# Performance work log

Measured on AMD Instinct MI355X. Metric: run time of the kernel, lower is better.

Reference implementation:

```python
import jax, jax.numpy as jnp
import numpy as np

B, C, H, W = 4, 320, 32, 32
HEADS = 8
LTXT, DCROSS = 77, 768
HW = H * W


def _ln(x, w, b, eps=1e-5):
    mu = x.mean(-1, keepdims=True)
    var = jnp.var(x, axis=-1, keepdims=True)
    return (x - mu) * jax.lax.rsqrt(var + eps) * w + b


def _gn(x, w, b, groups=32, eps=1e-6):
    Bx, Cx, Hx, Wx = x.shape
    xg = x.reshape(Bx, groups, -1)
    mu = xg.mean(-1, keepdims=True)
    var = jnp.var(xg, axis=-1, keepdims=True)
    xn = ((xg - mu) * jax.lax.rsqrt(var + eps)).reshape(Bx, Cx, Hx, Wx)
    return xn * w[None, :, None, None] + b[None, :, None, None]


def _attn(q, k, v, bias=None):
    Bq, S, Cd = q.shape
    dh = Cd // HEADS
    qh = q.reshape(Bq, S, HEADS, dh)
    kh = k.reshape(Bq, -1, HEADS, dh)
    vh = v.reshape(Bq, -1, HEADS, dh)
    s = jnp.einsum('bqhd,bkhd->bhqk', qh, kh) * (1.0 / np.sqrt(dh))
    if bias is not None:
        s = s + bias  # additive 0/1 otsu mask, exactly as the torch code passes it
    p = jax.nn.softmax(s, axis=-1)
    o = jnp.einsum('bhqk,bkhd->bqhd', p, vh).reshape(Bq, S, Cd)
    return o, p


def _block(x, ctx, prm, bias=None):
    # BasicTransformerBlock: self-attn -> cross-attn (returns probs) -> GEGLU FF
    (ln1w, ln1b, qkv, ow, ob, ln2w, ln2b, q2, kv2, o2w, o2b,
     ln3w, ln3b, ff1w, ff1b, ff2w, ff2b) = prm
    h = _ln(x, ln1w, ln1b)
    q, k, v = jnp.split(h @ qkv, 3, axis=-1)
    o, _ = _attn(q, k, v)
    x = x + o @ ow + ob
    h = _ln(x, ln2w, ln2b)
    k2, v2 = jnp.split(ctx @ kv2, 2, axis=-1)
    o2, p2 = _attn(h @ q2, k2, v2, bias)
    x = x + o2 @ o2w + o2b
    h = _ln(x, ln3w, ln3b)
    a, g = jnp.split(h @ ff1w + ff1b, 2, axis=-1)
    x = x + (a * jax.nn.gelu(g)) @ ff2w + ff2b
    return x, p2


def _otsu(m):
    # vectorized version of the 10-threshold otsu loop (m: [B/2, N])
    mn = m.min(-1, keepdims=True)
    mx = m.max(-1, keepdims=True)
    x = (m - mn) / (mx - mn)
    n = x.shape[-1]
    ts = jnp.arange(10, dtype=x.dtype) * 0.1  # thresholds t*0.1
    low = x[:, None, :] < ts[None, :, None]   # [B/2, 10, N]
    cnt_low = low.sum(-1).astype(x.dtype)
    cnt_high = n - cnt_low
    sum_low = jnp.where(low, x[:, None, :], 0.0).sum(-1)
    sum_high = x.sum(-1, keepdims=True) - sum_low
    mu_low = jnp.where(cnt_low > 0, sum_low / jnp.maximum(cnt_low, 1.0), jnp.nan)
    mu_high = jnp.where(cnt_high > 0, sum_high / jnp.maximum(cnt_high, 1.0), jnp.nan)
    g = (cnt_low / n) * (cnt_high / n) * (mu_low - mu_high) ** 2
    g = jnp.where(jnp.isnan(g), -jnp.inf, g)  # torch: nan > max_g is False -> skipped
    best = jnp.argmax(g, axis=-1)             # first max == torch strict-> ties keep earliest
    gmax = jnp.take_along_axis(g, best[:, None], axis=-1)[:, 0]
    thr = jnp.where(gmax > 0, best.astype(x.dtype) * 0.1, 0.0)[:, None]
    return jnp.where(x < thr, 0.0, jnp.where(x > thr, 1.0, x))


def _fwd(gn_w, gn_b, pin_w, pin_b,
         b_ln1w, b_ln1b, b_qkv, b_ow, b_ob, b_ln2w, b_ln2b, b_q2, b_kv2, b_o2w, b_o2b,
         b_ln3w, b_ln3b, b_ff1w, b_ff1b, b_ff2w, b_ff2b,
         i_ln1w, i_ln1b, i_qkv, i_ow, i_ob, i_ln2w, i_ln2b, i_q2, i_kv2, i_o2w, i_o2b,
         i_ln3w, i_ln3b, i_ff1w, i_ff1b, i_ff2w, i_ff2b,
         pout_w, pout_b, hidden_states, encoder_hidden_states,
         ph_b, ph_t, eot_b, eot_t):
    residual = hidden_states
    h = _gn(hidden_states, gn_w, gn_b)
    h = h.transpose(0, 2, 3, 1).reshape(B, HW, C)
    h = h @ pin_w + pin_b  # use_linear_projection path
    blk = (b_ln1w, b_ln1b, b_qkv, b_ow, b_ob, b_ln2w, b_ln2b, b_q2, b_kv2, b_o2w, b_o2b,
           b_ln3w, b_ln3b, b_ff1w, b_ff1b, b_ff2w, b_ff2b)
    iblk = (i_ln1w, i_ln1b, i_qkv, i_ow, i_ob, i_ln2w, i_ln2b, i_q2, i_kv2, i_o2w, i_o2b,
            i_ln3w, i_ln3b, i_ff1w, i_ff1b, i_ff2w, i_ff2b)
    h, probs = _block(h, encoder_hidden_states, blk)   # probs [B, heads, HW, 77]
    ap = probs.mean(1)[B // 2:]                        # head-avg attn_probs, cond half
    attn = ap.transpose(0, 2, 1)                       # [B/2, 77, HW]
    attn_ph = attn[ph_b, ph_t]                         # [B/2, HW]
    attn_eot = jax.lax.stop_gradient(attn[eot_b, eot_t])
    loss_reg = jnp.mean((attn_ph / attn_ph.max(-1, keepdims=True)
                         - attn_eot / attn_eot.max(-1, keepdims=True)) ** 2)
    mask = _otsu(jax.lax.stop_gradient(attn_ph))       # [B/2, HW]
    bias = mask[:, None, None, :]                      # broadcast over heads and queries
    hs, img = h[:B // 2], h[B // 2:]
    hs, _ = _block(hs, img, iblk, bias)                # image_cross_attention
    h = jnp.concatenate([hs, img], axis=0)
    h = h @ pout_w + pout_b
    sample = h.reshape(B, H, W, C).transpose(0, 3, 1, 2) + residual
    return sample, loss_reg


def setup_inputs():
    key = jax.random.key(0)
    ki = iter(jax.random.split(key, 80))
    f32 = jnp.float32

    def rn(shape, s=0.02):
        return jax.random.normal(next(ki), shape, f32) * s

    def blk(p, cross):
        return {p + 'ln1w': jnp.ones((C,), f32), p + 'ln1b': jnp.zeros((C,), f32),
                p + 'qkv': rn((C, 3 * C)), p + 'ow': rn((C, C)), p + 'ob': jnp.zeros((C,), f32),
                p + 'ln2w': jnp.ones((C,), f32), p + 'ln2b': jnp.zeros((C,), f32),
                p + 'q2': rn((C, C)), p + 'kv2': rn((cross, 2 * C)),
                p + 'o2w': rn((C, C)), p + 'o2b': jnp.zeros((C,), f32),
                p + 'ln3w': jnp.ones((C,), f32), p + 'ln3b': jnp.zeros((C,), f32),
                p + 'ff1w': rn((C, 8 * C)), p + 'ff1b': jnp.zeros((8 * C,), f32),
                p + 'ff2w': rn((4 * C, C)), p + 'ff2b': jnp.zeros((C,), f32)}

    inp = {'gn_w': jnp.ones((C,), f32), 'gn_b': jnp.zeros((C,), f32),
           'pin_w': rn((C, C)), 'pin_b': jnp.zeros((C,), f32)}
    inp.update(blk('b_', DCROSS))
    inp.update(blk('i_', C))
    inp['pout_w'] = rn((C, C))
    inp['pout_b'] = jnp.zeros((C,), f32)
    inp['hidden_states'] = jax.random.normal(next(ki), (B, C, H, W), f32)
    inp['encoder_hidden_states'] = jax.random.normal(next(ki), (B, LTXT, DCROSS), f32)
    inp['ph_b'] = jnp.arange(B // 2)
    inp['ph_t'] = jax.random.randint(next(ki), (B // 2,), 0, LTXT)
    inp['eot_b'] = jnp.arange(B // 2)
    inp['eot_t'] = jax.random.randint(next(ki), (B // 2,), 0, LTXT)
    return inp


def reference(gn_w, gn_b, pin_w, pin_b,
              b_ln1w, b_ln1b, b_qkv, b_ow, b_ob, b_ln2w, b_ln2b, b_q2, b_kv2, b_o2w, b_o2b,
              b_ln3w, b_ln3b, b_ff1w, b_ff1b, b_ff2w, b_ff2b,
              i_ln1w, i_ln1b, i_qkv, i_ow, i_ob, i_ln2w, i_ln2b, i_q2, i_kv2, i_o2w, i_o2b,
              i_ln3w, i_ln3b, i_ff1w, i_ff1b, i_ff2w, i_ff2b,
              pout_w, pout_b, hidden_states, encoder_hidden_states,
              ph_b, ph_t, eot_b, eot_t):
    return _fwd(gn_w, gn_b, pin_w, pin_b,
                b_ln1w, b_ln1b, b_qkv, b_ow, b_ob, b_ln2w, b_ln2b, b_q2, b_kv2, b_o2w, b_o2b,
                b_ln3w, b_ln3b, b_ff1w, b_ff1b, b_ff2w, b_ff2b,
                i_ln1w, i_ln1b, i_qkv, i_ow, i_ob, i_ln2w, i_ln2b, i_q2, i_kv2, i_o2w, i_o2b,
                i_ln3w, i_ln3b, i_ff1w, i_ff1b, i_ff2w, i_ff2b,
                pout_w, pout_b, hidden_states, encoder_hidden_states,
                ph_b, ph_t, eot_b, eot_t)
```

## Files before the change

### kernel.cpp

```cpp
#include <hip/hip_runtime.h>
#include <hip/hip_bf16.h>
#include <math.h>

#define NH 8
#define DH 40
#define CCH 320
#define SCALE 0.15811388300841897f

typedef __attribute__((ext_vector_type(8))) short short8;
typedef __attribute__((ext_vector_type(4))) float float4v;

static __device__ __forceinline__ unsigned short f2bf(float x) {
  __hip_bfloat16 t = __float2bfloat16(x);
  return *reinterpret_cast<unsigned short*>(&t);
}

static __device__ __forceinline__ void gload16(const void* g, void* l) {
  __builtin_amdgcn_global_load_lds((__attribute__((address_space(1))) void*)g,
                                   (__attribute__((address_space(3))) void*)l, 16, 0, 0);
}

__global__ __launch_bounds__(256) void gn_kernel(const float* __restrict__ x,
                                                 const float* __restrict__ w,
                                                 const float* __restrict__ b,
                                                 unsigned short* __restrict__ out) {
  int batch = blockIdx.x >> 5;
  int g = blockIdx.x & 31;
  const int CPG = 10;
  const float* xp = x + ((size_t)batch * CCH + g * CPG) * 1024;
  float s = 0.f, ss = 0.f;
  for (int i = threadIdx.x; i < CPG * 1024; i += 256) { float v = xp[i]; s += v; ss += v * v; }
  __shared__ float r1[256], r2[256];
  r1[threadIdx.x] = s; r2[threadIdx.x] = ss; __syncthreads();
  for (int off = 128; off > 0; off >>= 1) {
    if (threadIdx.x < off) { r1[threadIdx.x] += r1[threadIdx.x + off]; r2[threadIdx.x] += r2[threadIdx.x + off]; }
    __syncthreads();
  }
  float mu = r1[0] * (1.f / 10240.f);
  float var = r2[0] * (1.f / 10240.f) - mu * mu;
  float inv = rsqrtf(var + 1e-6f);
  for (int i = threadIdx.x; i < CPG * 1024; i += 256) {
    int ci = i >> 10; int hw = i & 1023; int c = g * CPG + ci;
    float v = (xp[i] - mu) * inv * w[c] + b[c];
    out[((size_t)batch * 1024 + hw) * CCH + c] = f2bf(v);
  }
}

__global__ __launch_bounds__(256) void ln_kernel(const float* __restrict__ x,
                                                 const float* __restrict__ w,
                                                 const float* __restrict__ b,
                                                 unsigned short* __restrict__ out, int M) {
  int row = blockIdx.x * 4 + (threadIdx.x >> 6);
  if (row >= M) return;
  const float* xp = x + (size_t)row * CCH;
  int lane = threadIdx.x & 63;
  float v[5]; float s = 0.f;
#pragma unroll
  for (int i = 0; i < 5; i++) { v[i] = xp[lane + 64 * i]; s += v[i]; }
#pragma unroll
  for (int o = 32; o > 0; o >>= 1) s += __shfl_xor(s, o);
  float mu = s * (1.f / 320.f);
  float ss = 0.f;
#pragma unroll
  for (int i = 0; i < 5; i++) { float d = v[i] - mu; ss += d * d; }
#pragma unroll
  for (int o = 32; o > 0; o >>= 1) ss += __shfl_xor(ss, o);
  float inv = rsqrtf(ss * (1.f / 320.f) + 1e-5f);
  unsigned short* op = out + (size_t)row * CCH;
#pragma unroll
  for (int i = 0; i < 5; i++) { int c = lane + 64 * i; op[c] = f2bf((v[i] - mu) * inv * w[c] + b[c]); }
}

struct WTab {
  const float* src[16];
  unsigned short* dst[16];
  int Kd[16];
  int Nd[16];
  int perm[16];
  int tstart[17];
  float* lz;
};
__global__ __launch_bounds__(256) void wconv_kernel(WTab t) {
  __shared__ float tile[32][33];
  if (blockIdx.x == 0 && threadIdx.x == 0) *t.lz = 0.f;
  int gid = blockIdx.x;
  int w = 0;
  while (w < 15 && gid >= t.tstart[w + 1]) w++;
  int local = gid - t.tstart[w];
  int K = t.Kd[w], N = t.Nd[w];
  int ntx = (N + 31) >> 5;
  int bx = local % ntx, by = local / ntx;
  int nb = bx * 32, kb = by * 32;
  const float* src = t.src[w];
  unsigned short* dst = t.dst[w];
  int doperm = t.perm[w];
  int half = N >> 1;
  int tx = threadIdx.x & 31, ty = threadIdx.x >> 5;
  for (int i = ty; i < 32; i += 8) {
    int k = kb + i, n = nb + tx;
    tile[i][tx] = (k < K && n < N) ? src[(size_t)k * N + n] : 0.f;
  }
  __syncthreads();
  for (int i = ty; i < 32; i += 8) {
    int n = nb + i, k = kb + tx;
    if (n < N && k < K) {
      int nd = n;
      if (doperm) {
        if (n < half) nd = (n >> 5) * 64 + (n & 31);
        else { int c = n - half; nd = (c >> 5) * 64 + 32 + (c & 31); }
      }
      dst[(size_t)nd * K + k] = f2bf(tile[tx][i]);
    }
  }
}

__global__ __launch_bounds__(256) void lngemm64_kernel(const float* __restrict__ A,
                                                       const float* __restrict__ lnw,
                                                       const float* __restrict__ lnb,
                                                       const unsigned short* __restrict__ Bt,
                                                       unsigned short* __restrict__ outp,
                                                       int M, int N) {
  __shared__ unsigned short As[64][328];
  __shared__ unsigned short Bsd[2][64][32];
  __shared__ float Wf[320], Bf[320];
  __shared__ float Mu[64], Iv[64];
  const int K = 320;
  int tid = threadIdx.x;
  int lane = tid & 63;
  int wv = tid >> 6;
  int quad = lane >> 4;
  int col = lane & 15;
  int m0 = blockIdx.y * 64;
  int n0 = blockIdx.x * 64;
  const unsigned short* bp0 = Bt + (size_t)(n0 + (tid >> 2)) * K + (tid & 3) * 8;
  gload16(bp0, ((char*)Bsd[0]) + wv * 1024);
  for (int i = tid; i < 320; i += 256) { Wf[i] = lnw[i]; Bf[i] = lnb[i]; }
  int l32 = tid & 31;
  int rsub = tid >> 5;
  for (int it = 0; it < 8; it++) {
    int r = it * 8 + rsub;
    const float* ap = A + (size_t)(m0 + r) * K;
    float s = 0.f, ss = 0.f;
#pragma unroll
    for (int j = 0; j < 10; j++) { float v = ap[l32 + j * 32]; s += v; ss += v * v; }
#pragma unroll
    for (int o = 16; o > 0; o >>= 1) { s += __shfl_xor(s, o); ss += __shfl_xor(ss, o); }
    if (l32 == 0) {
      float mu = s * (1.f / 320.f);
      Mu[r] = mu;
      Iv[r] = rsqrtf(ss * (1.f / 320.f) - mu * mu + 1e-5f);
    }
  }
  __syncthreads();
#pragma unroll 4
  for (int i = 0; i < 20; i++) {
    int cc = i * 256 + tid;
    int r = cc / 80, c4 = cc - r * 80;
    int c = c4 * 4;
    float4 v = *(const float4*)(A + (size_t)(m0 + r) * K + c);
    float mu = Mu[r], iv = Iv[r];
    ushort4 o;
    o.x = f2bf((v.x - mu) * iv * Wf[c] + Bf[c]);
    o.y = f2bf((v.y - mu) * iv * Wf[c + 1] + Bf[c + 1]);
    o.z = f2bf((v.z - mu) * iv * Wf[c + 2] + Bf[c + 2]);
    o.w = f2bf((v.w - mu) * iv * Wf[c + 3] + Bf[c + 3]);
    *(ushort4*)&As[r][c] = o;
  }
  __syncthreads();
  float4v acc[4];
  float4v zero = {0.f, 0.f, 0.f, 0.f};
#pragma unroll
  for (int j = 0; j < 4; j++) acc[j] = zero;
  for (int t = 0; t < 10; t++) {
    if (t < 9) gload16(bp0 + (t + 1) * 32, ((char*)Bsd[(t + 1) & 1]) + wv * 1024);
    int k0 = t * 32;
    short8 af = *(short8*)&As[wv * 16 + col][k0 + quad * 8];
#pragma unroll
    for (int j = 0; j < 4; j++) {
      short8 bfr = *(short8*)&Bsd[t & 1][j * 16 + col][quad * 8];
      acc[j] = __builtin_amdgcn_mfma_f32_16x16x32_bf16(af, bfr, acc[j], 0, 0, 0);
    }
    __syncthreads();
  }
#pragma unroll
  for (int j = 0; j < 4; j++) {
    int n = n0 + j * 16 + col;
#pragma unroll
    for (int r = 0; r < 4; r++) {
      int m = m0 + wv * 16 + quad * 4 + r;
      outp[(size_t)m * N + n] = f2bf(acc[j][r]);
    }
  }
}

__global__ __launch_bounds__(256) void mergegemm64_kernel(const float* __restrict__ Opart,
                                                          const float* __restrict__ mpart,
                                                          const float* __restrict__ lpart,
                                                          const unsigned short* __restrict__ Bt,
                                                          const float* __restrict__ bias,
                                                          float* __restrict__ h, int M) {
  __shared__ unsigned short As[64][328];
  __shared__ unsigned short Bsd[2][64][32];
  const int K = 320;
  int tid = threadIdx.x;
  int lane = tid & 63;
  int wv = tid >> 6;
  int quad = lane >> 4;
  int col = lane & 15;
  int m0 = blockIdx.y * 64;
  int n0 = blockIdx.x * 64;
  const unsigned short* bp0 = Bt + (size_t)(n0 + (tid >> 2)) * K + (tid & 3) * 8;
  gload16(bp0, ((char*)Bsd[0]) + wv * 1024);
#pragma unroll
  for (int i = 0; i < 10; i++) {
    int cc = i * 256 + tid;
    int r = cc / 40, c8 = cc - r * 40;
    int c = c8 * 8;
    int hh = c / 40;
    int d = c - hh * 40;
    int m = m0 + r, b = m >> 10, q = m & 1023;
    size_t ri = ((size_t)(b * NH + hh) * 1024 + q) * 4;
    float ma = mpart[ri], mb = mpart[ri + 1], mc = mpart[ri + 2], md = mpart[ri + 3];
    float Mx = fmaxf(fmaxf(ma, mb), fmaxf(mc, md));
    float w0 = __expf(ma - Mx), w1 = __expf(mb - Mx), w2 = __expf(mc - Mx), w3 = __expf(md - Mx);
    float L = lpart[ri] * w0 + lpart[ri + 1] * w1 + lpart[ri + 2] * w2 + lpart[ri + 3] * w3;
    float inv = 1.f / L;
    w0 *= inv; w1 *= inv; w2 *= inv; w3 *= inv;
    const float* p0 = Opart + (ri + 0) * DH + d;
    const float* p1 = Opart + (ri + 1) * DH + d;
    const float* p2 = Opart + (ri + 2) * DH + d;
    const float* p3 = Opart + (ri + 3) * DH + d;
    float4 a0 = *(const float4*)p0, a1 = *(const float4*)p1, a2 = *(const float4*)p2, a3 = *(const float4*)p3;
    float4 b0 = *(const float4*)(p0 + 4), b1 = *(const float4*)(p1 + 4), b2 = *(const float4*)(p2 + 4), b3 = *(const float4*)(p3 + 4);
    ushort4 u0, u1;
    u0.x = f2bf(a0.x * w0 + a1.x * w1 + a2.x * w2 + a3.x * w3);
    u0.y = f2bf(a0.y * w0 + a1.y * w1 + a2.y * w2 + a3.y * w3);
    u0.z = f2bf(a0.z * w0 + a1.z * w1 + a2.z * w2 + a3.z * w3);
    u0.w = f2bf(a0.w * w0 + a1.w * w1 + a2.w * w2 + a3.w * w3);
    u1.x = f2bf(b0.x * w0 + b1.x * w1 + b2.x * w2 + b3.x * w3);
    u1.y = f2bf(b0.y * w0 + b1.y * w1 + b2.y * w2 + b3.y * w3);
    u1.z = f2bf(b0.z * w0 + b1.z * w1 + b2.z * w2 + b3.z * w3);
    u1.w = f2bf(b0.w * w0 + b1.w * w1 + b2.w * w2 + b3.w * w3);
    *(ushort4*)&As[r][c] = u0;
    *(ushort4*)&As[r][c + 4] = u1;
  }
  __syncthreads();
  float4v acc[4];
  float4v zero = {0.f, 0.f, 0.f, 0.f};
#pragma unroll
  for (int j = 0; j < 4; j++) acc[j] = zero;
  for (int t = 0; t < 10; t++) {
    if (t < 9) gload16(bp0 + (t + 1) * 32, ((char*)Bsd[(t + 1) & 1]) + wv * 1024);
    int k0 = t * 32;
    short8 af = *(short8*)&As[wv * 16 + col][k0 + quad * 8];
#pragma unroll
    for (int j = 0; j < 4; j++) {
      short8 bfr = *(short8*)&Bsd[t & 1][j * 16 + col][quad * 8];
      acc[j] = __builtin_amdgcn_mfma_f32_16x16x32_bf16(af, bfr, acc[j], 0, 0, 0);
    }
    __syncthreads();
  }
#pragma unroll
  for (int j = 0; j < 4; j++) {
    int n = n0 + j * 16 + col;
    float bv = bias[n];
#pragma unroll
    for (int r = 0; r < 4; r++) {
      int m = m0 + wv * 16 + quad * 4 + r;
      size_t oi = (size_t)m * 320 + n;
      h[oi] = acc[j][r] + bv + h[oi];
    }
  }
}

__global__ __launch_bounds__(256) void mgemm64_kernel(const void* __restrict__ Ap,
                                                      const unsigned short* __restrict__ Bt,
                                                      const float* __restrict__ bias,
                                                      const float* __restrict__ res,
                                                      void* __restrict__ outp,
                                                      void* __restrict__ outp2,
                                                      int M, int N, int K, int a32, int omode) {
  __shared__ unsigned short As[64][160];
  __shared__ unsigned short Bs[64][160];
  int tid = threadIdx.x;
  int lane = tid & 63;
  int wv = tid >> 6;
  int quad = lane >> 4;
  int col = lane & 15;
  int m0 = blockIdx.y * 64;
  int n0 = blockIdx.x * 64;
  float4v acc[4];
  float4v zero = {0.f, 0.f, 0.f, 0.f};
#pragma unroll
  for (int j = 0; j < 4; j++) acc[j] = zero;
  short8 vzero = {0, 0, 0, 0, 0, 0, 0, 0};
  int kfast = (!a32) && ((K % 160) == 0);
  int off[5];
#pragma unroll
  for (int i = 0; i < 5; i++) { int c = i * 256 + tid; int row = c / 20; off[i] = row * K + (c - row * 20) * 8; }
  int wb = (tid & 192) * 16;
  const unsigned short* Ab = (const unsigned short*)Ap + (size_t)m0 * K;
  const unsigned short* Bb = Bt + (size_t)n0 * K;
  for (int k0 = 0; k0 < K; k0 += 160) {
    if (kfast) {
#pragma unroll
      for (int i = 0; i < 5; i++) {
        gload16(Ab + off[i] + k0, ((char*)As) + wb + i * 4096);
        gload16(Bb + off[i] + k0, ((char*)Bs) + wb + i * 4096);
      }
    } else {
#pragma unroll
      for (int i = 0; i < 5; i++) {
        int u = tid + i * 256;
        int row = u / 20, seg = u - row * 20;
        int k = k0 + seg * 8;
        int m = m0 + row;
        short8 av = vzero;
        if (m < M && k < K) {
          if (a32) {
            const float* Af = (const float*)Ap;
            float4 f0 = *(const float4*)(Af + (size_t)m * K + k);
            float4 f1 = *(const float4*)(Af + (size_t)m * K + k + 4);
            av[0] = (short)f2bf(f0.x); av[1] = (short)f2bf(f0.y);
            av[2] = (short)f2bf(f0.z); av[3] = (short)f2bf(f0.w);
            av[4] = (short)f2bf(f1.x); av[5] = (short)f2bf(f1.y);
            av[6] = (short)f2bf(f1.z); av[7] = (short)f2bf(f1.w);
          } else {
            av = *(const short8*)((const unsigned short*)Ap + (size_t)m * K + k);
          }
        }
        *(short8*)&As[row][seg * 8] = av;
        int n = n0 + row;
        short8 bv = vzero;
        if (n < N && k < K) bv = *(const short8*)(Bt + (size_t)n * K + k);
        *(short8*)&Bs[row][seg * 8] = bv;
      }
    }
    __syncthreads();
#pragma unroll
    for (int kk = 0; kk < 5; kk++) {
      int kq2 = kk * 32 + quad * 8;
      short8 af = *(short8*)&As[wv * 16 + col][kq2];
#pragma unroll
      for (int j = 0; j < 4; j++) {
        short8 bfr = *(short8*)&Bs[j * 16 + col][kq2];
        acc[j] = __builtin_amdgcn_mfma_f32_16x16x32_bf16(af, bfr, acc[j], 0, 0, 0);
      }
    }
    __syncthreads();
  }
  if (omode == 3) {
    int half = N >> 1;
#pragma unroll
    for (int jb = 0; jb < 2; jb++) {
      int nout = (n0 >> 1) + jb * 16 + col;
      float ba = bias[nout];
      float bg = bias[half + nout];
#pragma unroll
      for (int r = 0; r < 4; r++) {
        int m = m0 + wv * 16 + quad * 4 + r;
        if (m < M) {
          float a = acc[jb][r] + ba;
          float g = acc[jb + 2][r] + bg;
          float t2 = tanhf(0.7978845608028654f * (g + 0.044715f * g * g * g));
          ((unsigned short*)outp)[(size_t)m * half + nout] = f2bf(a * (0.5f * g * (1.f + t2)));
        }
      }
    }
    return;
  }
#pragma unroll
  for (int j = 0; j < 4; j++) {
    int n = n0 + j * 16 + col;
    if (n >= N) continue;
    float bv = bias ? bias[n] : 0.f;
#pragma unroll
    for (int r = 0; r < 4; r++) {
      int m = m0 + wv * 16 + quad * 4 + r;
      if (m < M) {
        float v = acc[j][r] + bv;
        if (omode == 2) {
          int bq = m >> 10, hw = m & 1023;
          size_t oi = ((size_t)bq * N + n) * 1024 + hw;
          ((float*)outp)[oi] = v + res[oi];
        } else {
          if (res) v += res[(size_t)m * N + n];
          if (omode == 1) ((unsigned short*)outp)[(size_t)m * N + n] = f2bf(v);
          else {
            ((float*)outp)[(size_t)m * N + n] = v;
            if (omode == 4) ((unsigned short*)outp2)[(size_t)m * N + n] = f2bf(v);
          }
        }
      }
    }
  }
}

#define VSTR 72
__global__ __launch_bounds__(256) void mfattns_kernel(const unsigned short* __restrict__ qp, int qstr,
                                                      const unsigned short* __restrict__ kp, int kstr,
                                                      const unsigned short* __restrict__ vp, int vstr,
                                                      const float* __restrict__ bias,
                                                      float* __restrict__ Opart,
                                                      float* __restrict__ mpart,
                                                      float* __restrict__ lpart) {
  __shared__ unsigned short Ks[64 * 56];
  __shared__ unsigned short Vt[48 * VSTR];
  __shared__ unsigned short Ps[4][16 * 72];
  int tid = threadIdx.x;
  int lane = tid & 63;
  int wv = tid >> 6;
  int quad = lane >> 4;
  int col = lane & 15;
  int bid = blockIdx.x;
  int split = bid & 3;
  int qt = (bid >> 2) & 15;
  int h = (bid >> 6) & 7;
  int b = bid >> 9;

  short8 zero8 = {0, 0, 0, 0, 0, 0, 0, 0};
  int qrow = qt * 64 + wv * 16 + col;
  const unsigned short* qbase = qp + (size_t)(b * 1024 + qrow) * qstr + h * DH;
  short8 qf0 = *(const short8*)(qbase + quad * 8);
  short8 qf1 = (quad == 0) ? *(const short8*)(qbase + 32) : zero8;

  float4v Oacc[3];
  float4v fzero = {0.f, 0.f, 0.f, 0.f};
  Oacc[0] = fzero; Oacc[1] = fzero; Oacc[2] = fzero;
  float mr[4] = {-3.4e38f, -3.4e38f, -3.4e38f, -3.4e38f};
  float lr[4] = {0.f, 0.f, 0.f, 0.f};

  for (int kt = split * 4; kt < split * 4 + 4; kt++) {
    int kb = kt * 64;
    __syncthreads();
    for (int u = tid; u < 384; u += 256) {
      int key = u / 6, s = u - key * 6;
      short8 kv8 = zero8;
      if (s < 5) kv8 = *(const short8*)(kp + (size_t)(b * 1024 + kb + key) * kstr + h * DH + s * 8);
      *(short8*)&Ks[key * 56 + s * 8] = kv8;
    }
    for (int u = tid; u < 384; u += 256) {
      int s = u >> 6, key = u & 63;
      short8 vv8 = zero8;
      if (s < 5) vv8 = *(const short8*)(vp + (size_t)(b * 1024 + kb + key) * vstr + h * DH + s * 8);
#pragma unroll
      for (int j = 0; j < 8; j++) Vt[(s * 8 + j) * VSTR + key] = (unsigned short)vv8[j];
    }
    __syncthreads();

    float4v sf[4];
#pragma unroll
    for (int jb = 0; jb < 4; jb++) {
      const unsigned short* krow = &Ks[(jb * 16 + col) * 56];
      short8 bk0 = *(const short8*)(krow + quad * 8);
      short8 bk1 = (quad == 0) ? *(const short8*)(krow + 32) : zero8;
      float4v s = fzero;
      s = __builtin_amdgcn_mfma_f32_16x16x32_bf16(qf0, bk0, s, 0, 0, 0);
      s = __builtin_amdgcn_mfma_f32_16x16x32_bf16(qf1, bk1, s, 0, 0, 0);
      float bv = bias ? bias[b * 1024 + kb + jb * 16 + col] : 0.f;
#pragma unroll
      for (int r = 0; r < 4; r++) s[r] = s[r] * SCALE + bv;
      sf[jb] = s;
    }
    float tmax[4];
#pragma unroll
    for (int r = 0; r < 4; r++) {
      float t = fmaxf(fmaxf(sf[0][r], sf[1][r]), fmaxf(sf[2][r], sf[3][r]));
#pragma unroll
      for (int o = 1; o < 16; o <<= 1) t = fmaxf(t, __shfl_xor(t, o));
      tmax[r] = t;
    }
    float al[4];
#pragma unroll
    for (int r = 0; r < 4; r++) {
      float mnew = fmaxf(mr[r], tmax[r]);
      al[r] = __expf(mr[r] - mnew);
      mr[r] = mnew;
      lr[r] *= al[r];
    }
#pragma unroll
    for (int nb = 0; nb < 3; nb++)
#pragma unroll
      for (int r = 0; r < 4; r++) Oacc[nb][r] *= al[r];
    float rs[4] = {0.f, 0.f, 0.f, 0.f};
#pragma unroll
    for (int jb = 0; jb < 4; jb++) {
#pragma unroll
      for (int r = 0; r < 4; r++) {
        float p = __expf(sf[jb][r] - mr[r]);
        rs[r] += p;
        Ps[wv][(quad * 4 + r) * 72 + jb * 16 + col] = f2bf(p);
      }
    }
#pragma unroll
    for (int r = 0; r < 4; r++) {
      float t = rs[r];
#pragma unroll
      for (int o = 1; o < 16; o <<= 1) t += __shfl_xor(t, o);
      lr[r] += t;
    }
#pragma unroll
    for (int kc = 0; kc < 2; kc++) {
      int koff = kc * 32 + quad * 8;
      short8 pa = *(const short8*)&Ps[wv][col * 72 + koff];
#pragma unroll
      for (int nb = 0; nb < 3; nb++) {
        short8 vb = *(const short8*)&Vt[(nb * 16 + col) * VSTR + koff];
        Oacc[nb] = __builtin_amdgcn_mfma_f32_16x16x32_bf16(pa, vb, Oacc[nb], 0, 0, 0);
      }
    }
  }
#pragma unroll
  for (int r = 0; r < 4; r++) {
    int qo = qt * 64 + wv * 16 + quad * 4 + r;
    size_t rowidx = (size_t)(b * NH + h) * 1024 + qo;
    float* orow = Opart + (rowidx * 4 + split) * DH;
#pragma unroll
    for (int nb = 0; nb < 3; nb++) {
      int d = nb * 16 + col;
      if (d < DH) orow[d] = Oacc[nb][r];
    }
    if (col == 0) {
      mpart[rowidx * 4 + split] = mr[r];
      lpart[rowidx * 4 + split] = lr[r];
    }
  }
}

#define CVSTR 104
__global__ __launch_bounds__(256) void cattnm_kernel(const unsigned short* __restrict__ qp,
                                                     const unsigned short* __restrict__ kvp,
                                                     unsigned short* __restrict__ op,
                                                     float* __restrict__ probs) {
  __shared__ unsigned short Ks[80 * 56];
  __shared__ unsigned short Vt[48 * CVSTR];
  __shared__ unsigned short Ps[4][16 * 104];
  int tid = threadIdx.x;
  int lane = tid & 63;
  int wv = tid >> 6;
  int quad = lane >> 4;
  int col = lane & 15;
  int bid = blockIdx.x;
  int qt = bid & 15;
  int h = (bid >> 4) & 7;
  int b = bid >> 7;

  short8 zero8 = {0, 0, 0, 0, 0, 0, 0, 0};
  for (int u = tid; u < 480; u += 256) {
    int key = u / 6, s = u - key * 6;
    short8 v8 = zero8;
    if (s < 5 && key < 77) v8 = *(const short8*)(kvp + (size_t)(b * 77 + key) * 640 + h * DH + s * 8);
    *(short8*)&Ks[key * 56 + s * 8] = v8;
  }
  for (int u = tid; u < 576; u += 256) {
    int s = u / 96, key = u - s * 96;
    short8 v8 = zero8;
    if (s < 5 && key < 77) v8 = *(const short8*)(kvp + (size_t)(b * 77 + key) * 640 + 320 + h * DH + s * 8);
#pragma unroll
    for (int j = 0; j < 8; j++) Vt[(s * 8 + j) * CVSTR + key] = (unsigned short)v8[j];
  }
  int qrow = qt * 64 + wv * 16 + col;
  const unsigned short* qbase = qp + (size_t)(b * 1024 + qrow) * CCH + h * DH;
  short8 qf0 = *(const short8*)(qbase + quad * 8);
  short8 qf1 = (quad == 0) ? *(const short8*)(qbase + 32) : zero8;
  __syncthreads();

  float4v fzero = {0.f, 0.f, 0.f, 0.f};
  float4v sf[5];
#pragma unroll
  for (int jb = 0; jb < 5; jb++) {
    const unsigned short* krow = &Ks[(jb * 16 + col) * 56];
    short8 bk0 = *(const short8*)(krow + quad * 8);
    short8 bk1 = (quad == 0) ? *(const short8*)(krow + 32) : zero8;
    float4v s = fzero;
    s = __builtin_amdgcn_mfma_f32_16x16x32_bf16(qf0, bk0, s, 0, 0, 0);
    s = __builtin_amdgcn_mfma_f32_16x16x32_bf16(qf1, bk1, s, 0, 0, 0);
    int key = jb * 16 + col;
    float msk = (key < 77) ? 0.f : -3.4e38f;
#pragma unroll
    for (int r = 0; r < 4; r++) s[r] = s[r] * SCALE + msk;
    sf[jb] = s;
  }
  float inv[4];
#pragma unroll
  for (int r = 0; r < 4; r++) {
    float t = sf[0][r];
#pragma unroll
    for (int jb = 1; jb < 5; jb++) t = fmaxf(t, sf[jb][r]);
#pragma unroll
    for (int o = 1; o < 16; o <<= 1) t = fmaxf(t, __shfl_xor(t, o));
    float sum = 0.f;
#pragma unroll
    for (int jb = 0; jb < 5; jb++) { float e = __expf(sf[jb][r] - t); sf[jb][r] = e; sum += e; }
#pragma unroll
    for (int o = 1; o < 16; o <<= 1) sum += __shfl_xor(sum, o);
    inv[r] = 1.f / sum;
  }
#pragma unroll
  for (int jb = 0; jb < 5; jb++) {
    int key = jb * 16 + col;
    float4v pv;
#pragma unroll
    for (int r = 0; r < 4; r++) {
      float p = sf[jb][r] * inv[r];
      Ps[wv][(quad * 4 + r) * 104 + jb * 16 + col] = f2bf(p);
      pv[r] = p;
    }
    if (b >= 2 && key < 77) {
      size_t pi = ((size_t)((b - 2) * NH + h) * 77 + key) * 1024 + qt * 64 + wv * 16 + quad * 4;
      *(float4v*)&probs[pi] = pv;
    }
  }
  float4v Oacc[3];
  Oacc[0] = fzero; Oacc[1] = fzero; Oacc[2] = fzero;
#pragma unroll
  for (int kc = 0; kc < 3; kc++) {
    int koff = kc * 32 + quad * 8;
    short8 pa = (koff < 80) ? *(const short8*)&Ps[wv][col * 104 + koff] : zero8;
#pragma unroll
    for (int nb = 0; nb < 3; nb++) {
      short8 vb = *(const short8*)&Vt[(nb * 16 + col) * CVSTR + koff];
      Oacc[nb] = __builtin_amdgcn_mfma_f32_16x16x32_bf16(pa, vb, Oacc[nb], 0, 0, 0);
    }
  }
#pragma unroll
  for (int r = 0; r < 4; r++) {
    int qo = qt * 64 + wv * 16 + quad * 4 + r;
    unsigned short* orow = op + (size_t)(b * 1024 + qo) * CCH + h * DH;
#pragma unroll
    for (int nb = 0; nb < 3; nb++) {
      int d = nb * 16 + col;
      if (d < DH) orow[d] = f2bf(Oacc[nb][r]);
    }
  }
}

__global__ __launch_bounds__(256) void eol_kernel(const float* __restrict__ pT,
                                                  const int* __restrict__ phb, const int* __restrict__ pht,
                                                  const int* __restrict__ eob, const int* __restrict__ eot,
                                                  float* __restrict__ mask,
                                                  float* __restrict__ lossout) {
  __shared__ float S[4][24];
  __shared__ float shthr;
  int i = blockIdx.x, tid = threadIdx.x;
  int lane = tid & 63, wv = tid >> 6;
  int pb = phb[i], pt = pht[i], eb = eob[i], et = eot[i];
  float x[4], y[4];
#pragma unroll
  for (int j = 0; j < 4; j++) {
    int q = tid + 256 * j;
    float s1 = 0.f, s2 = 0.f;
#pragma unroll
    for (int hh = 0; hh < NH; hh++) {
      s1 += pT[((size_t)(pb * NH + hh) * 77 + pt) * 1024 + q];
      s2 += pT[((size_t)(eb * NH + hh) * 77 + et) * 1024 + q];
    }
    x[j] = s1 * 0.125f;
    y[j] = s2 * 0.125f;
  }
  float mx = fmaxf(fmaxf(x[0], x[1]), fmaxf(x[2], x[3]));
  float me = fmaxf(fmaxf(y[0], y[1]), fmaxf(y[2], y[3]));
  float mn = fminf(fminf(x[0], x[1]), fminf(x[2], x[3]));
  float sx = x[0] + x[1] + x[2] + x[3];
#pragma unroll
  for (int o = 32; o > 0; o >>= 1) {
    mx = fmaxf(mx, __shfl_xor(mx, o));
    me = fmaxf(me, __shfl_xor(me, o));
    mn = fminf(mn, __shfl_xor(mn, o));
    sx += __shfl_xor(sx, o);
  }
  if (lane == 0) { S[wv][0] = mx; S[wv][1] = me; S[wv][2] = mn; S[wv][3] = sx; }
  __syncthreads();
  mx = fmaxf(fmaxf(S[0][0], S[1][0]), fmaxf(S[2][0], S[3][0]));
  me = fmaxf(fmaxf(S[0][1], S[1][1]), fmaxf(S[2][1], S[3][1]));
  mn = fminf(fminf(S[0][2], S[1][2]), fminf(S[2][2], S[3][2]));
  sx = S[0][3] + S[1][3] + S[2][3] + S[3][3];
  float invmp = 1.f / mx, invme = 1.f / me;
  float inv = 1.f / (mx - mn);
  float lp = 0.f;
  float cnt[10], sm[10];
#pragma unroll
  for (int t = 0; t < 10; t++) { cnt[t] = 0.f; sm[t] = 0.f; }
#pragma unroll
  for (int j = 0; j < 4; j++) {
    float d = x[j] * invmp - y[j] * invme;
    lp += d * d;
    float v = (x[j] - mn) * inv;
#pragma unroll
    for (int t = 0; t < 10; t++) {
      if (v < t * 0.1f) { cnt[t] += 1.f; sm[t] += v; }
    }
  }
#pragma unroll
  for (int o = 32; o > 0; o >>= 1) {
    lp += __shfl_xor(lp, o);
#pragma unroll
    for (int t = 0; t < 10; t++) { cnt[t] += __shfl_xor(cnt[t], o); sm[t] += __shfl_xor(sm[t], o); }
  }
  __syncthreads();
  if (lane == 0) {
    S[wv][0] = lp;
#pragma unroll
    for (int t = 0; t < 10; t++) { S[wv][1 + t] = cnt[t]; S[wv][11 + t] = sm[t]; }
  }
  __syncthreads();
  if (tid == 0) {
    float lpt = S[0][0] + S[1][0] + S[2][0] + S[3][0];
    atomicAdd(lossout, lpt * (1.f / 2048.f));
    float total = (sx - 1024.f * mn) * inv;
    float gmax = -3.4e38f; int best = 0;
    for (int t = 0; t < 10; t++) {
      float c_low = S[0][1 + t] + S[1][1 + t] + S[2][1 + t] + S[3][1 + t];
      float s_low = S[0][11 + t] + S[1][11 + t] + S[2][11 + t] + S[3][11 + t];
      float c_high = 1024.f - c_low;
      float g;
      if (c_low > 0.f && c_high > 0.f) {
        float mu_l = s_low / c_low;
        float mu_h = (total - s_low) / c_high;
        float dd = mu_l - mu_h;
        g = (c_low * (1.f / 1024.f)) * (c_high * (1.f / 1024.f)) * dd * dd;
      } else g = -3.4e38f;
      if (g > gmax) { gmax = g; best = t; }
    }
    shthr = (gmax > 0.f) ? best * 0.1f : 0.f;
  }
  __syncthreads();
  float thr = shthr;
#pragma unroll
  for (int j = 0; j < 4; j++) {
    int q = tid + 256 * j;
    float v = (x[j] - mn) * inv;
    mask[i * 1024 + q] = (v < thr) ? 0.f : ((v > thr) ? 1.f : v);
  }
}

extern "C" void kernel_launch(void* const* d_in, const int* in_sizes, int n_in,
                              void* d_out, int out_size, void* d_ws, size_t ws_size,
                              hipStream_t stream) {
  auto F = [&](int i) { return (const float*)d_in[i]; };
  auto I = [&](int i) { return (const int*)d_in[i]; };

  float* ws = (float*)d_ws;
  float* h    = ws;
  float* ffb  = h    + 1310720;
  float* p2   = ffb  + 10485760;
  float* mask = p2   + 2523136;

  float* Opart = ffb;
  float* mpart = ffb + 5242880;
  float* lpart = ffb + 5242880 + 131072;

  unsigned short* b16   = (unsigned short*)(mask + 2048);
  unsigned short* lnb16 = b16;
  unsigned short* attb16= lnb16 + 1310720;
  unsigned short* actb16= attb16 + 1310720;
  unsigned short* qkv16 = actb16 + 5242880;
  unsigned short* q16   = qkv16 + 3932160;
  unsigned short* kv16  = q16 + 1310720;
  unsigned short* hb16  = kv16 + 1310720;
  unsigned short* wptr  = hb16 + 1310720;

  auto walloc = [&](int n) { unsigned short* p = wptr; wptr += n; return p; };
  unsigned short* pin_t  = walloc(102400);
  unsigned short* bqkv_t = walloc(307200);
  unsigned short* bow_t  = walloc(102400);
  unsigned short* bq2_t  = walloc(102400);
  unsigned short* bkv2_t = walloc(491520);
  unsigned short* bo2_t  = walloc(102400);
  unsigned short* bff1_t = walloc(819200);
  unsigned short* bff2_t = walloc(409600);
  unsigned short* iqkv_t = walloc(307200);
  unsigned short* iow_t  = walloc(102400);
  unsigned short* iq2_t  = walloc(102400);
  unsigned short* ikv2_t = walloc(204800);
  unsigned short* io2_t  = walloc(102400);
  unsigned short* iff1_t = walloc(819200);
  unsigned short* iff2_t = walloc(409600);
  unsigned short* pout_t = walloc(102400);

  float* out = (float*)d_out;

  WTab wt;
  wt.lz = out + 1310720;
  int nt = 0, cnt = 0;
  auto addw = [&](const float* s, unsigned short* d, int K, int N, int perm) {
    wt.src[cnt] = s; wt.dst[cnt] = d; wt.Kd[cnt] = K; wt.Nd[cnt] = N; wt.perm[cnt] = perm;
    wt.tstart[cnt] = nt;
    nt += ((K + 31) / 32) * ((N + 31) / 32);
    cnt++;
  };
  addw(F(2), pin_t, 320, 320, 0);
  addw(F(4 + 2), bqkv_t, 320, 960, 0);
  addw(F(4 + 3), bow_t, 320, 320, 0);
  addw(F(4 + 7), bq2_t, 320, 320, 0);
  addw(F(4 + 8), bkv2_t, 768, 640, 0);
  addw(F(4 + 9), bo2_t, 320, 320, 0);
  addw(F(4 + 13), bff1_t, 320, 2560, 1);
  addw(F(4 + 15), bff2_t, 1280, 320, 0);
  addw(F(21 + 2), iqkv_t, 320, 960, 0);
  addw(F(21 + 3), iow_t, 320, 320, 0);
  addw(F(21 + 7), iq2_t, 320, 320, 0);
  addw(F(21 + 8), ikv2_t, 320, 640, 0);
  addw(F(21 + 9), io2_t, 320, 320, 0);
  addw(F(21 + 13), iff1_t, 320, 2560, 1);
  addw(F(21 + 15), iff2_t, 1280, 320, 0);
  addw(F(38), pout_t, 320, 320, 0);
  wt.tstart[16] = nt;

  wconv_kernel<<<nt, 256, 0, stream>>>(wt);

  auto gemm64 = [&](const void* A, const unsigned short* Wt, const float* bias,
                    const float* res, void* o, int M, int N, int K, int a32, int omode,
                    void* o2 = nullptr) {
    dim3 g((N + 63) / 64, (M + 63) / 64);
    mgemm64_kernel<<<g, 256, 0, stream>>>(A, Wt, bias, res, o, o2, M, N, K, a32, omode);
  };
  auto lngemm = [&](const float* A, const float* lw, const float* lb,
                    const unsigned short* Wt, unsigned short* o, int M, int N) {
    dim3 g(N / 64, M / 64);
    lngemm64_kernel<<<g, 256, 0, stream>>>(A, lw, lb, Wt, o, M, N);
  };
  auto mergegemm = [&](const unsigned short* Wt, const float* bias, int M) {
    dim3 g(5, M / 64);
    mergegemm64_kernel<<<g, 256, 0, stream>>>(Opart, mpart, lpart, Wt, bias, h, M);
  };

  gn_kernel<<<128, 256, 0, stream>>>(F(40), F(0), F(1), lnb16);
  gemm64(lnb16, pin_t, F(3), nullptr, h, 4096, 320, 320, 0, 0);

  auto run_block = [&](int p, int Bx, bool img_block,
                       const unsigned short* qkv_t, const unsigned short* ow_t,
                       const unsigned short* q2_t, const unsigned short* kv2_t,
                       const unsigned short* o2_t, const unsigned short* ff1_t,
                       const unsigned short* ff2_t) {
    int M = Bx * 1024;
    ln_kernel<<<M / 4, 256, 0, stream>>>(h, F(p + 0), F(p + 1), lnb16, M);
    gemm64(lnb16, qkv_t, nullptr, nullptr, qkv16, M, 960, 320, 0, 1);
    mfattns_kernel<<<Bx * 512, 256, 0, stream>>>(qkv16, 960, qkv16 + 320, 960, qkv16 + 640, 960,
                                                 nullptr, Opart, mpart, lpart);
    mergegemm(ow_t, F(p + 4), M);
    lngemm(h, F(p + 5), F(p + 6), q2_t, q16, M, 320);
    if (!img_block) {
      gemm64(F(41), kv2_t, nullptr, nullptr, kv16, Bx * 77, 640, 768, 1, 1);
      cattnm_kernel<<<Bx * 128, 256, 0, stream>>>(q16, kv16, attb16, p2);
      gemm64(attb16, o2_t, F(p + 10), h, h, M, 320, 320, 0, 0);
    } else {
      gemm64(hb16 + (size_t)2 * 1024 * 320, kv2_t, nullptr, nullptr, kv16, Bx * 1024, 640, 320, 0, 1);
      mfattns_kernel<<<Bx * 512, 256, 0, stream>>>(q16, 320, kv16, 640, kv16 + 320, 640,
                                                   mask, Opart, mpart, lpart);
      mergegemm(o2_t, F(p + 10), M);
    }
    ln_kernel<<<M / 4, 256, 0, stream>>>(h, F(p + 11), F(p + 12), lnb16, M);
    gemm64(lnb16, ff1_t, F(p + 14), nullptr, actb16, M, 2560, 320, 0, 3);
    gemm64(actb16, ff2_t, F(p + 16), h, h, M, 320, 1280, 0, 4, hb16);
  };

  run_block(4, 4, false, bqkv_t, bow_t, bq2_t, bkv2_t, bo2_t, bff1_t, bff2_t);

  eol_kernel<<<2, 256, 0, stream>>>(p2, I(42), I(43), I(44), I(45), mask, out + 1310720);

  run_block(21, 2, true, iqkv_t, iow_t, iq2_t, ikv2_t, io2_t, iff1_t, iff2_t);

  gemm64(hb16, pout_t, F(39), F(40), out, 4096, 320, 320, 0, 2);
}
```

Measured before the change: 527.8 us.

## Use base-2 softmax with lazy rescaling and split merge from out-projection GEMM

```diff
diff --git a/kernel.cpp b/kernel.cpp
--- a/kernel.cpp
+++ b/kernel.cpp
@@ -6,6 +6,8 @@
 #define DH 40
 #define CCH 320
 #define SCALE 0.15811388300841897f
+#define SCL2 0.22810857f
+#define LOG2E 1.44269504f
 
 typedef __attribute__((ext_vector_type(8))) short short8;
 typedef __attribute__((ext_vector_type(4))) float float4v;
@@ -193,83 +195,35 @@
   }
 }
 
-__global__ __launch_bounds__(256) void mergegemm64_kernel(const float* __restrict__ Opart,
-                                                          const float* __restrict__ mpart,
-                                                          const float* __restrict__ lpart,
-                                                          const unsigned short* __restrict__ Bt,
-                                                          const float* __restrict__ bias,
-                                                          float* __restrict__ h, int M) {
-  __shared__ unsigned short As[64][328];
-  __shared__ unsigned short Bsd[2][64][32];
-  const int K = 320;
-  int tid = threadIdx.x;
-  int lane = tid & 63;
-  int wv = tid >> 6;
-  int quad = lane >> 4;
-  int col = lane & 15;
-  int m0 = blockIdx.y * 64;
-  int n0 = blockIdx.x * 64;
-  const unsigned short* bp0 = Bt + (size_t)(n0 + (tid >> 2)) * K + (tid & 3) * 8;
-  gload16(bp0, ((char*)Bsd[0]) + wv * 1024);
-#pragma unroll
-  for (int i = 0; i < 10; i++) {
-    int cc = i * 256 + tid;
-    int r = cc / 40, c8 = cc - r * 40;
-    int c = c8 * 8;
-    int hh = c / 40;
-    int d = c - hh * 40;
-    int m = m0 + r, b = m >> 10, q = m & 1023;
-    size_t ri = ((size_t)(b * NH + hh) * 1024 + q) * 4;
-    float ma = mpart[ri], mb = mpart[ri + 1], mc = mpart[ri + 2], md = mpart[ri + 3];
-    float Mx = fmaxf(fmaxf(ma, mb), fmaxf(mc, md));
-    float w0 = __expf(ma - Mx), w1 = __expf(mb - Mx), w2 = __expf(mc - Mx), w3 = __expf(md - Mx);
-    float L = lpart[ri] * w0 + lpart[ri + 1] * w1 + lpart[ri + 2] * w2 + lpart[ri + 3] * w3;
-    float inv = 1.f / L;
-    w0 *= inv; w1 *= inv; w2 *= inv; w3 *= inv;
-    const float* p0 = Opart + (ri + 0) * DH + d;
-    const float* p1 = Opart + (ri + 1) * DH + d;
-    const float* p2 = Opart + (ri + 2) * DH + d;
-    const float* p3 = Opart + (ri + 3) * DH + d;
-    float4 a0 = *(const float4*)p0, a1 = *(const float4*)p1, a2 = *(const float4*)p2, a3 = *(const float4*)p3;
-    float4 b0 = *(const float4*)(p0 + 4), b1 = *(const float4*)(p1 + 4), b2 = *(const float4*)(p2 + 4), b3 = *(const float4*)(p3 + 4);
-    ushort4 u0, u1;
-    u0.x = f2bf(a0.x * w0 + a1.x * w1 + a2.x * w2 + a3.x * w3);
-    u0.y = f2bf(a0.y * w0 + a1.y * w1 + a2.y * w2 + a3.y * w3);
-    u0.z = f2bf(a0.z * w0 + a1.z * w1 + a2.z * w2 + a3.z * w3);
-    u0.w = f2bf(a0.w * w0 + a1.w * w1 + a2.w * w2 + a3.w * w3);
-    u1.x = f2bf(b0.x * w0 + b1.x * w1 + b2.x * w2 + b3.x * w3);
-    u1.y = f2bf(b0.y * w0 + b1.y * w1 + b2.y * w2 + b3.y * w3);
-    u1.z = f2bf(b0.z * w0 + b1.z * w1 + b2.z * w2 + b3.z * w3);
-    u1.w = f2bf(b0.w * w0 + b1.w * w1 + b2.w * w2 + b3.w * w3);
-    *(ushort4*)&As[r][c] = u0;
-    *(ushort4*)&As[r][c + 4] = u1;
-  }
-  __syncthreads();
-  float4v acc[4];
-  float4v zero = {0.f, 0.f, 0.f, 0.f};
-#pragma unroll
-  for (int j = 0; j < 4; j++) acc[j] = zero;
-  for (int t = 0; t < 10; t++) {
-    if (t < 9) gload16(bp0 + (t + 1) * 32, ((char*)Bsd[(t + 1) & 1]) + wv * 1024);
-    int k0 = t * 32;
-    short8 af = *(short8*)&As[wv * 16 + col][k0 + quad * 8];
-#pragma unroll
-    for (int j = 0; j < 4; j++) {
-      short8 bfr = *(short8*)&Bsd[t & 1][j * 16 + col][quad * 8];
-      acc[j] = __builtin_amdgcn_mfma_f32_16x16x32_bf16(af, bfr, acc[j], 0, 0, 0);
-    }
-    __syncthreads();
-  }
-#pragma unroll
-  for (int j = 0; j < 4; j++) {
-    int n = n0 + j * 16 + col;
-    float bv = bias[n];
-#pragma unroll
-    for (int r = 0; r < 4; r++) {
-      int m = m0 + wv * 16 + quad * 4 + r;
-      size_t oi = (size_t)m * 320 + n;
-      h[oi] = acc[j][r] + bv + h[oi];
-    }
+__global__ __launch_bounds__(256) void merge_kernel(const float* __restrict__ Opart,
+                                                    const float* __restrict__ mpart,
+                                                    const float* __restrict__ lpart,
+                                                    unsigned short* __restrict__ op, int rows) {
+  int r = blockIdx.x * 256 + threadIdx.x;
+  if (r >= rows) return;
+  float m0 = mpart[r * 4 + 0], m1 = mpart[r * 4 + 1], m2 = mpart[r * 4 + 2], m3 = mpart[r * 4 + 3];
+  float M = fmaxf(fmaxf(m0, m1), fmaxf(m2, m3));
+  float w0 = exp2f(m0 - M), w1 = exp2f(m1 - M), w2 = exp2f(m2 - M), w3 = exp2f(m3 - M);
+  float L = lpart[r * 4 + 0] * w0 + lpart[r * 4 + 1] * w1 + lpart[r * 4 + 2] * w2 + lpart[r * 4 + 3] * w3;
+  float inv = 1.f / L;
+  w0 *= inv; w1 *= inv; w2 *= inv; w3 *= inv;
+  int q = r & 1023;
+  int h = (r >> 10) & 7;
+  int b = r >> 13;
+  const float4* p0 = (const float4*)(Opart + (size_t)(r * 4 + 0) * DH);
+  const float4* p1 = (const float4*)(Opart + (size_t)(r * 4 + 1) * DH);
+  const float4* p2 = (const float4*)(Opart + (size_t)(r * 4 + 2) * DH);
+  const float4* p3 = (const float4*)(Opart + (size_t)(r * 4 + 3) * DH);
+  unsigned short* o = op + ((size_t)(b * 1024 + q)) * 320 + h * DH;
+#pragma unroll
+  for (int j = 0; j < 10; j++) {
+    float4 a = p0[j], bb = p1[j], c = p2[j], d = p3[j];
+    ushort4 pk;
+    pk.x = f2bf(a.x * w0 + bb.x * w1 + c.x * w2 + d.x * w3);
+    pk.y = f2bf(a.y * w0 + bb.y * w1 + c.y * w2 + d.y * w3);
+    pk.z = f2bf(a.z * w0 + bb.z * w1 + c.z * w2 + d.z * w3);
+    pk.w = f2bf(a.w * w0 + bb.w * w1 + c.w * w2 + d.w * w3);
+    *(ushort4*)(o + j * 4) = pk;
   }
 }
 
@@ -429,6 +383,7 @@
   Oacc[0] = fzero; Oacc[1] = fzero; Oacc[2] = fzero;
   float mr[4] = {-3.4e38f, -3.4e38f, -3.4e38f, -3.4e38f};
   float lr[4] = {0.f, 0.f, 0.f, 0.f};
+  const float* biasb = bias ? (bias + b * 1024) : nullptr;
 
   for (int kt = split * 4; kt < split * 4 + 4; kt++) {
     int kb = kt * 64;
@@ -457,9 +412,9 @@
       float4v s = fzero;
       s = __builtin_amdgcn_mfma_f32_16x16x32_bf16(qf0, bk0, s, 0, 0, 0);
       s = __builtin_amdgcn_mfma_f32_16x16x32_bf16(qf1, bk1, s, 0, 0, 0);
-      float bv = bias ? bias[b * 1024 + kb + jb * 16 + col] : 0.f;
-#pragma unroll
-      for (int r = 0; r < 4; r++) s[r] = s[r] * SCALE + bv;
+      float bv = biasb ? biasb[kb + jb * 16 + col] * LOG2E : 0.f;
+#pragma unroll
+      for (int r = 0; r < 4; r++) s[r] = s[r] * SCL2 + bv;
       sf[jb] = s;
     }
     float tmax[4];
@@ -470,24 +425,28 @@
       for (int o = 1; o < 16; o <<= 1) t = fmaxf(t, __shfl_xor(t, o));
       tmax[r] = t;
     }
-    float al[4];
-#pragma unroll
-    for (int r = 0; r < 4; r++) {
-      float mnew = fmaxf(mr[r], tmax[r]);
-      al[r] = __expf(mr[r] - mnew);
-      mr[r] = mnew;
-      lr[r] *= al[r];
-    }
-#pragma unroll
-    for (int nb = 0; nb < 3; nb++)
-#pragma unroll
-      for (int r = 0; r < 4; r++) Oacc[nb][r] *= al[r];
+    float grow = fmaxf(fmaxf(tmax[0] - mr[0], tmax[1] - mr[1]),
+                       fmaxf(tmax[2] - mr[2], tmax[3] - mr[3]));
+    if (!__all(grow <= 8.f)) {
+      float al[4];
+#pragma unroll
+      for (int r = 0; r < 4; r++) {
+        float mnew = fmaxf(mr[r], tmax[r]);
+        al[r] = exp2f(mr[r] - mnew);
+        mr[r] = mnew;
+        lr[r] *= al[r];
+      }
+#pragma unroll
+      for (int nb = 0; nb < 3; nb++)
+#pragma unroll
+        for (int r = 0; r < 4; r++) Oacc[nb][r] *= al[r];
+    }
     float rs[4] = {0.f, 0.f, 0.f, 0.f};
 #pragma unroll
     for (int jb = 0; jb < 4; jb++) {
 #pragma unroll
       for (int r = 0; r < 4; r++) {
-        float p = __expf(sf[jb][r] - mr[r]);
+        float p = exp2f(sf[jb][r] - mr[r]);
         rs[r] += p;
         Ps[wv][(quad * 4 + r) * 72 + jb * 16 + col] = f2bf(p);
       }
@@ -578,7 +537,7 @@
     int key = jb * 16 + col;
     float msk = (key < 77) ? 0.f : -3.4e38f;
 #pragma unroll
-    for (int r = 0; r < 4; r++) s[r] = s[r] * SCALE + msk;
+    for (int r = 0; r < 4; r++) s[r] = s[r] * SCL2 + msk;
     sf[jb] = s;
   }
   float inv[4];
@@ -591,7 +550,7 @@
     for (int o = 1; o < 16; o <<= 1) t = fmaxf(t, __shfl_xor(t, o));
     float sum = 0.f;
 #pragma unroll
-    for (int jb = 0; jb < 5; jb++) { float e = __expf(sf[jb][r] - t); sf[jb][r] = e; sum += e; }
+    for (int jb = 0; jb < 5; jb++) { float e = exp2f(sf[jb][r] - t); sf[jb][r] = e; sum += e; }
 #pragma unroll
     for (int o = 1; o < 16; o <<= 1) sum += __shfl_xor(sum, o);
     inv[r] = 1.f / sum;
@@ -820,10 +779,6 @@
     dim3 g(N / 64, M / 64);
     lngemm64_kernel<<<g, 256, 0, stream>>>(A, lw, lb, Wt, o, M, N);
   };
-  auto mergegemm = [&](const unsigned short* Wt, const float* bias, int M) {
-    dim3 g(5, M / 64);
-    mergegemm64_kernel<<<g, 256, 0, stream>>>(Opart, mpart, lpart, Wt, bias, h, M);
-  };
 
   gn_kernel<<<128, 256, 0, stream>>>(F(40), F(0), F(1), lnb16);
   gemm64(lnb16, pin_t, F(3), nullptr, h, 4096, 320, 320, 0, 0);
@@ -838,7 +793,8 @@
     gemm64(lnb16, qkv_t, nullptr, nullptr, qkv16, M, 960, 320, 0, 1);
     mfattns_kernel<<<Bx * 512, 256, 0, stream>>>(qkv16, 960, qkv16 + 320, 960, qkv16 + 640, 960,
                                                  nullptr, Opart, mpart, lpart);
-    mergegemm(ow_t, F(p + 4), M);
+    merge_kernel<<<Bx * 32, 256, 0, stream>>>(Opart, mpart, lpart, attb16, Bx * 8192);
+    gemm64(attb16, ow_t, F(p + 4), h, h, M, 320, 320, 0, 0);
     lngemm(h, F(p + 5), F(p + 6), q2_t, q16, M, 320);
     if (!img_block) {
       gemm64(F(41), kv2_t, nullptr, nullptr, kv16, Bx * 77, 640, 768, 1, 1);
@@ -848,7 +804,8 @@
       gemm64(hb16 + (size_t)2 * 1024 * 320, kv2_t, nullptr, nullptr, kv16, Bx * 1024, 640, 320, 0, 1);
       mfattns_kernel<<<Bx * 512, 256, 0, stream>>>(q16, 320, kv16, 640, kv16 + 320, 640,
                                                    mask, Opart, mpart, lpart);
-      mergegemm(o2_t, F(p + 10), M);
+      merge_kernel<<<Bx * 32, 256, 0, stream>>>(Opart, mpart, lpart, attb16, Bx * 8192);
+      gemm64(attb16, o2_t, F(p + 10), h, h, M, 320, 320, 0, 0);
     }
     ln_kernel<<<M / 4, 256, 0, stream>>>(h, F(p + 11), F(p + 12), lnb16, M);
     gemm64(lnb16, ff1_t, F(p + 14), nullptr, actb16, M, 2560, 320, 0, 3);
```

Result: slower. 549.4 us (+4.1%).
